# Kernel tuning notes

Measured on AMD Instinct MI355X. Metric: run time of the kernel, lower is better.

Reference implementation:

```python
import jax, jax.numpy as jnp
import jax.scipy.linalg as jsp
import numpy as np

# Problem dimensions (match init_kwargs P_shape/A_shape)
N = 256   # variables
M = 512   # constraints
B = 64    # batch

# OSQP ADMM hyper-parameters (fixed-rho variant of the OSQP algorithm)
SIGMA = 1e-6
RHO = 0.1
ALPHA = 1.6
N_ITERS = 500


def setup_inputs() -> dict:
    key = jax.random.key(0)
    kP, kq, kA, kc = jax.random.split(key, 4)
    # P is diagonal with strictly positive entries -> PSD (values are the nnz of P)
    P_val = jax.random.uniform(kP, (B, N), dtype=jnp.float32) + 0.1
    q_val = jax.random.normal(kq, (B, N), dtype=jnp.float32)
    # A is a dense pattern; values stored row-major as its nnz vector
    A_val = jax.random.normal(kA, (B, M * N), dtype=jnp.float32) / np.sqrt(N)
    # Feasible box: l <= u by construction
    center = jax.random.normal(kc, (B, M), dtype=jnp.float32)
    l_val = center - 1.0
    u_val = center + 1.0
    return {"P_val": P_val, "q_val": q_val, "A_val": A_val, "l_val": l_val, "u_val": u_val}


def _admm_qp(P_val, q_val, A_val, l_val, u_val):
    """Batched OSQP-style ADMM solve of min 1/2 x'Px + q'x  s.t. l <= Ax <= u.

    P is diagonal (nnz pattern = diag), A is dense (nnz pattern = full m x n).
    """
    A = A_val.reshape(B, M, N)                      # [B,m,n]
    # KKT-like matrix M_k = P + sigma*I + rho*A'A   [B,n,n]
    eye = jnp.eye(N, dtype=P_val.dtype)
    P_diag = P_val + SIGMA                          # diagonal of P + sigma*I
    Mk = RHO * jnp.einsum('bmi,bmj->bij', A, A) + jax.vmap(jnp.diag)(P_diag)
    L = jnp.linalg.cholesky(Mk)                     # [B,n,n], factor once, reuse
    Lt = jnp.swapaxes(L, -1, -2)

    def kkt_solve(rhs):                             # rhs [B,n]
        y1 = jsp.solve_triangular(L, rhs[..., None], lower=True)
        y2 = jsp.solve_triangular(Lt, y1, lower=False)
        return y2[..., 0]

    x0 = jnp.zeros((B, N), dtype=P_val.dtype)
    z0 = jnp.zeros((B, M), dtype=P_val.dtype)
    y0 = jnp.zeros((B, M), dtype=P_val.dtype)

    def step(state, _):
        x, z, y = state
        rhs = SIGMA * x - q_val + jnp.einsum('bmn,bm->bn', A, RHO * z - y)
        x_t = kkt_solve(rhs)                        # x-tilde
        z_t = jnp.einsum('bmn,bn->bm', A, x_t)      # z-tilde = A x_t
        x_new = ALPHA * x_t + (1.0 - ALPHA) * x
        z_hat = ALPHA * z_t + (1.0 - ALPHA) * z
        z_new = jnp.clip(z_hat + y / RHO, l_val, u_val)
        y_new = y + RHO * (z_hat - z_new)
        return (x_new, z_new, y_new), None

    (x, _, _), _ = jax.lax.scan(step, (x0, z0, y0), None, length=N_ITERS)
    return x


def reference(P_val, q_val, A_val, l_val, u_val):
    return _admm_qp(P_val, q_val, A_val, l_val, u_val)   # [B, n] primal solutions
```

## Files before the change

### kernel.cpp

```cpp
#include <hip/hip_runtime.h>
#include <hip/hip_fp16.h>

#define N_VAR 256
#define M_CON 512
#define BATCH 64
#define SIGMA_C 1e-6f
#define RHO_C 0.1f
#define ALPHA_C 1.6f
#define NITERS 500

__global__ __launch_bounds__(256) void k_transpose(const float* __restrict__ A,
                                                   float* __restrict__ At) {
  __shared__ float tile[32][33];
  int b = blockIdx.z;
  int n0 = blockIdx.x * 32;
  int m0 = blockIdx.y * 32;
  const float* Ab = A + (size_t)b * (M_CON * N_VAR);
  float* Atb = At + (size_t)b * (M_CON * N_VAR);
  int tx = threadIdx.x, ty = threadIdx.y;
#pragma unroll
  for (int j = 0; j < 32; j += 8)
    tile[ty + j][tx] = Ab[(size_t)(m0 + ty + j) * N_VAR + n0 + tx];
  __syncthreads();
#pragma unroll
  for (int j = 0; j < 32; j += 8)
    Atb[(size_t)(n0 + ty + j) * M_CON + m0 + tx] = tile[tx][ty + j];
}

__global__ __launch_bounds__(256) void k_ntgemm(
    const float* __restrict__ X, const float* __restrict__ Y,
    float* __restrict__ C, int I, int J, int K,
    long long bsX, long long bsY, long long bsC, float alpha,
    const float* __restrict__ diagv, int tilesJ) {
  int b = blockIdx.y;
  int ti = blockIdx.x / tilesJ, tj = blockIdx.x % tilesJ;
  int i0 = ti * 128, j0 = tj * 128;
  const float* Xb = X + (size_t)b * bsX;
  const float* Yb = Y + (size_t)b * bsY;
  float* Cb = C + (size_t)b * bsC;
  __shared__ float Xs[16][128];
  __shared__ float Ys[16][128];
  int tid = threadIdx.x;
  int tx = tid & 15, ty = tid >> 4;
  float acc[8][8];
#pragma unroll
  for (int r = 0; r < 8; ++r)
#pragma unroll
    for (int c = 0; c < 8; ++c) acc[r][c] = 0.0f;

  for (int kk = 0; kk < K; kk += 16) {
#pragma unroll
    for (int v = 0; v < 2; ++v) {
      int idx = v * 256 + tid;
      int row = idx >> 2;
      int k4 = (idx & 3) * 4;
      float4 gx = *(const float4*)(Xb + (size_t)(i0 + row) * K + kk + k4);
      Xs[k4 + 0][row] = gx.x; Xs[k4 + 1][row] = gx.y;
      Xs[k4 + 2][row] = gx.z; Xs[k4 + 3][row] = gx.w;
      float4 gy = *(const float4*)(Yb + (size_t)(j0 + row) * K + kk + k4);
      Ys[k4 + 0][row] = gy.x; Ys[k4 + 1][row] = gy.y;
      Ys[k4 + 2][row] = gy.z; Ys[k4 + 3][row] = gy.w;
    }
    __syncthreads();
#pragma unroll
    for (int k = 0; k < 16; ++k) {
      float xr[8], yr[8];
      *(float4*)&xr[0] = *(float4*)&Xs[k][ty * 8];
      *(float4*)&xr[4] = *(float4*)&Xs[k][ty * 8 + 4];
      *(float4*)&yr[0] = *(float4*)&Ys[k][tx * 8];
      *(float4*)&yr[4] = *(float4*)&Ys[k][tx * 8 + 4];
#pragma unroll
      for (int r = 0; r < 8; ++r)
#pragma unroll
        for (int c = 0; c < 8; ++c) acc[r][c] += xr[r] * yr[c];
    }
    __syncthreads();
  }
#pragma unroll
  for (int r = 0; r < 8; ++r) {
    int gi = i0 + ty * 8 + r;
#pragma unroll
    for (int c = 0; c < 8; ++c) {
      int gj = j0 + tx * 8 + c;
      float val = acc[r][c] * alpha;
      if (diagv != nullptr && gi == gj) val += diagv[(size_t)b * N_VAR + gi] + SIGMA_C;
      Cb[(size_t)gi * J + gj] = val;
    }
  }
}

__global__ __launch_bounds__(512, 2) void k_invert(const float* __restrict__ Mk,
                                                   float* __restrict__ Mi) {
  int b = blockIdx.x;
  const float* src = Mk + (size_t)b * 65536;
  float* dst = Mi + (size_t)b * 65536;
  int t = threadIdx.x;
  int c = t & 255, rh = t >> 8;

  float a[128];
#pragma unroll
  for (int j = 0; j < 128; ++j) a[j] = src[(size_t)(rh * 128 + j) * 256 + c];

  __shared__ float colPan[256][8];
  __shared__ float rowPan[2][8][260];
  __shared__ float PiSh[64];
  __shared__ float Rp[8][260];

  int rh_s = __builtin_amdgcn_readfirstlane(rh);
  int cw_s = __builtin_amdgcn_readfirstlane((t >> 6) & 3);

  if (rh == 0) {
#pragma unroll
    for (int j = 0; j < 8; ++j) rowPan[0][j][c] = a[j];
  }
  __syncthreads();

  for (int s = 0; s < 32; ++s) {
    int kb = s * 8;
    int cur = s & 1, nxt = cur ^ 1;
    int kh = kb >> 7, kj = kb & 127;
    int khn = (kb + 8) >> 7, kjn = (kb + 8) & 127;
    bool mycol = (c >= kb) && (c < kb + 8);

    if (cw_s == (kb >> 6)) {
      if (mycol) {
        int f = c - kb;
#pragma unroll
        for (int j = 0; j < 128; ++j) colPan[rh * 128 + j][f] = a[j];
      }
    }
    if (t < 64) {
      int e = t >> 3, f = t & 7;
      float p = rowPan[cur][e][kb + f];
#pragma unroll
      for (int k2 = 0; k2 < 8; ++k2) {
        float piv = __shfl(p, k2 * 8 + k2);
        float rv = __shfl(p, k2 * 8 + f);
        float cv = __shfl(p, e * 8 + k2);
        float pivinv = 1.0f / piv;
        float srv = rv * pivinv;
        float gen = p - cv * srv;
        p = gen;
        if (e == k2) p = srv;
        if (f == k2) p = -cv * pivinv;
        if (e == k2 && f == k2) p = pivinv;
      }
      PiSh[t] = p;
    }
    __syncthreads();

    float rpan[8];
#pragma unroll
    for (int f2 = 0; f2 < 8; ++f2) rpan[f2] = rowPan[cur][f2][c];
    float rp[8];
#pragma unroll
    for (int e = 0; e < 8; ++e) {
      float4 p0 = *(const float4*)&PiSh[e * 8];
      float4 p1 = *(const float4*)&PiSh[e * 8 + 4];
      rp[e] = p0.x * rpan[0] + p0.y * rpan[1] + p0.z * rpan[2] + p0.w * rpan[3] +
              p1.x * rpan[4] + p1.y * rpan[5] + p1.z * rpan[6] + p1.w * rpan[7];
    }
    if (cw_s == (kb >> 6)) {
      if (mycol) {
        int f = c - kb;
#pragma unroll
        for (int e = 0; e < 8; ++e) rp[e] = PiSh[e * 8 + f];
      }
    }
#pragma unroll
    for (int e = 0; e < 8; ++e) Rp[e][c] = rp[e];

    bool myhalfk = (rh_s == kh);
    bool stashw = (s != 31) && (rh_s == khn);
#pragma unroll
    for (int j = 0; j < 128; ++j) {
      float4 c0 = *(const float4*)&colPan[rh * 128 + j][0];
      float4 c1 = *(const float4*)&colPan[rh * 128 + j][4];
      float aold = a[j];
      float nv = aold -
                 (c0.x * rp[0] + c0.y * rp[1] + c0.z * rp[2] + c0.w * rp[3] +
                  c1.x * rp[4] + c1.y * rp[5] + c1.z * rp[6] + c1.w * rp[7]);
      if (mycol) nv -= aold;
      if (myhalfk && j >= kj && j < kj + 8)
        nv = Rp[j - kj][c];
      a[j] = nv;
      if (stashw && j >= kjn && j < kjn + 8)
        rowPan[nxt][j - kjn][c] = nv;
    }
    __syncthreads();
  }

#pragma unroll
  for (int j = 0; j < 128; ++j) dst[(size_t)(rh * 128 + j) * 256 + c] = a[j];
}

__global__ __launch_bounds__(256) void k_matvec_h(const float* __restrict__ Mi,
                                                  const float* __restrict__ q,
                                                  float* __restrict__ h) {
  int b = blockIdx.x, t = threadIdx.x;
  __shared__ float qs[256];
  qs[t] = q[(size_t)b * 256 + t];
  __syncthreads();
  const float* Mb = Mi + (size_t)b * 65536;
  float acc = 0.0f;
  for (int k = 0; k < 256; ++k) acc += Mb[(size_t)k * 256 + t] * qs[k];
  h[(size_t)b * 256 + t] = acc;
}

__global__ __launch_bounds__(512) void k_matvec_d(const float* __restrict__ At,
                                                  const float* __restrict__ h,
                                                  float* __restrict__ d) {
  int b = blockIdx.x, t = threadIdx.x;
  __shared__ float hs[256];
  if (t < 256) hs[t] = h[(size_t)b * 256 + t];
  __syncthreads();
  const float* Ab = At + (size_t)b * 131072;
  float acc = 0.0f;
  for (int n = 0; n < 256; ++n) acc += Ab[(size_t)n * 512 + t] * hs[n];
  d[(size_t)b * 512 + t] = acc;
}

__global__ __launch_bounds__(512, 2) void k_admm4(
    const float* __restrict__ G, const float* __restrict__ dvec,
    const float* __restrict__ lv, const float* __restrict__ uv,
    unsigned long long* __restrict__ wtag, float* __restrict__ Sbuf) {
  int g = blockIdx.x;
  int b = (g & 7) + 8 * ((g >> 3) & 7);
  int s = g >> 6;
  int t = threadIdx.x;
  int l = t & 63, wv = t >> 6;
  int c0 = wv * 64;

  __shared__ __align__(16) float wbuf[8][64];
  __shared__ float part[2][8][128];

  const float* Gb = G + (size_t)b * 262144;
  const float* g0p = Gb + (size_t)(s * 128 + l) * 512 + c0;
  const float* g1p = Gb + (size_t)(s * 128 + 64 + l) * 512 + c0;
  float G0[64], G1[64];
#pragma unroll
  for (int j = 0; j < 16; ++j) {
    float4 v0 = *(const float4*)(g0p + 4 * j);
    G0[4 * j + 0] = v0.x; G0[4 * j + 1] = v0.y;
    G0[4 * j + 2] = v0.z; G0[4 * j + 3] = v0.w;
    float4 v1 = *(const float4*)(g1p + 4 * j);
    G1[4 * j + 0] = v1.x; G1[4 * j + 1] = v1.y;
    G1[4 * j + 2] = v1.z; G1[4 * j + 3] = v1.w;
  }

  float zreg = 0.0f, yreg = 0.0f, Sreg = 0.0f;
  float lreg = 0.0f, ureg = 0.0f, dreg = 0.0f;
  if (t < 128) {
    lreg = lv[(size_t)b * 512 + s * 128 + t];
    ureg = uv[(size_t)b * 512 + s * 128 + t];
    dreg = dvec[(size_t)b * 512 + s * 128 + t];
  }
  wbuf[wv][l] = 0.0f;

  unsigned long long* wt0 = wtag + (size_t)b * 512;
  unsigned long long* wt1 = wtag + 32768 + (size_t)b * 512;
  const float4* wq4 = (const float4*)(wbuf[wv]);

  for (int it = 0; it < NITERS; ++it) {
    if (it > 0) {
      unsigned long long* wp = (it & 1) ? wt1 : wt0;
      unsigned want = (unsigned)it;
      unsigned long long v;
      for (;;) {
        v = __hip_atomic_load(&wp[c0 + l], __ATOMIC_RELAXED,
                              __HIP_MEMORY_SCOPE_AGENT);
        if (__all((unsigned)(v >> 32) == want)) break;
        __builtin_amdgcn_s_sleep(1);
      }
      wbuf[wv][l] = __uint_as_float((unsigned)(v & 0xffffffffu));
    }

    float r0a = 0.f, r0b = 0.f, r1a = 0.f, r1b = 0.f;
#pragma unroll
    for (int j = 0; j < 8; ++j) {
      float4 wa = wq4[2 * j];
      float4 wc = wq4[2 * j + 1];
      r0a += G0[8 * j + 0] * wa.x + G0[8 * j + 1] * wa.y +
             G0[8 * j + 2] * wa.z + G0[8 * j + 3] * wa.w;
      r1a += G1[8 * j + 0] * wa.x + G1[8 * j + 1] * wa.y +
             G1[8 * j + 2] * wa.z + G1[8 * j + 3] * wa.w;
      r0b += G0[8 * j + 4] * wc.x + G0[8 * j + 5] * wc.y +
             G0[8 * j + 6] * wc.z + G0[8 * j + 7] * wc.w;
      r1b += G1[8 * j + 4] * wc.x + G1[8 * j + 5] * wc.y +
             G1[8 * j + 6] * wc.z + G1[8 * j + 7] * wc.w;
    }
    int pp = it & 1;
    part[pp][wv][l] = r0a + r0b;
    part[pp][wv][64 + l] = r1a + r1b;
    __syncthreads();

    if (t < 128) {
      float w_old = RHO_C * zreg - yreg;
      Sreg = w_old - 0.6f * Sreg;
      float p = part[pp][0][t] + part[pp][1][t] + part[pp][2][t] +
                part[pp][3][t] + part[pp][4][t] + part[pp][5][t] +
                part[pp][6][t] + part[pp][7][t];
      float zt = p - dreg;
      float zh = ALPHA_C * zt + (1.0f - ALPHA_C) * zreg;
      float zc = zh + yreg * (1.0f / RHO_C);
      zc = fminf(fmaxf(zc, lreg), ureg);
      yreg += RHO_C * (zh - zc);
      zreg = zc;
      if (it < NITERS - 1) {
        float wn = RHO_C * zreg - yreg;
        unsigned long long pk =
            ((unsigned long long)(unsigned)(it + 1) << 32) |
            (unsigned long long)__float_as_uint(wn);
        unsigned long long* wp = ((it + 1) & 1) ? wt1 : wt0;
        __hip_atomic_store(&wp[s * 128 + t], pk, __ATOMIC_RELAXED,
                           __HIP_MEMORY_SCOPE_AGENT);
      }
    }
  }

  if (t < 128) Sbuf[(size_t)b * 512 + s * 128 + t] = Sreg;
}

__global__ __launch_bounds__(256) void k_final(
    const float* __restrict__ A, const float* __restrict__ q,
    const float* __restrict__ Mi, const float* __restrict__ Sbuf,
    float* __restrict__ xout) {
  int b = blockIdx.x, t = threadIdx.x;
  __shared__ float Ssh[512];
  __shared__ float uu[256];
  for (int i = t; i < 512; i += 256) Ssh[i] = Sbuf[(size_t)b * 512 + i];
  __syncthreads();
  const float* Ab = A + (size_t)b * 131072;
  float acc = 0.0f;
  for (int m = 0; m < 512; ++m) acc += Ab[(size_t)m * 256 + t] * Ssh[m];
  uu[t] = ALPHA_C * acc - q[(size_t)b * 256 + t];
  __syncthreads();
  const float* Mb = Mi + (size_t)b * 65536;
  float x = 0.0f;
  for (int kk = 0; kk < 256; ++kk) x += Mb[(size_t)kk * 256 + t] * uu[kk];
  xout[(size_t)b * 256 + t] = x;
}

extern "C" void kernel_launch(void* const* d_in, const int* in_sizes, int n_in,
                              void* d_out, int out_size, void* d_ws, size_t ws_size,
                              hipStream_t stream) {
  (void)in_sizes; (void)n_in; (void)out_size; (void)ws_size;
  const float* P = (const float*)d_in[0];
  const float* q = (const float*)d_in[1];
  const float* Av = (const float*)d_in[2];
  const float* lv = (const float*)d_in[3];
  const float* uv = (const float*)d_in[4];
  float* xout = (float*)d_out;

  float* ws = (float*)d_ws;
  float* At = ws;
  float* F  = ws;
  float* Mi = ws + 8388608;
  float* Mk = ws + 12582912;
  float* G  = ws + 12582912;
  float* hv = ws + 29360128;
  float* dv = ws + 29376512;
  float* Sbuf = ws + 29409280;
  unsigned long long* wtag = (unsigned long long*)ws;

  k_transpose<<<dim3(8, 16, 64), dim3(32, 8), 0, stream>>>(Av, At);
  k_ntgemm<<<dim3(4, 64), 256, 0, stream>>>(At, At, Mk, 256, 256, 512,
                                            131072LL, 131072LL, 65536LL,
                                            RHO_C, P, 2);
  k_invert<<<64, 512, 0, stream>>>(Mk, Mi);
  k_matvec_h<<<64, 256, 0, stream>>>(Mi, q, hv);
  k_matvec_d<<<64, 512, 0, stream>>>(At, hv, dv);
  k_ntgemm<<<dim3(8, 64), 256, 0, stream>>>(Av, Mi, F, 512, 256, 256,
                                            131072LL, 65536LL, 131072LL,
                                            1.0f, nullptr, 2);
  k_ntgemm<<<dim3(16, 64), 256, 0, stream>>>(F, Av, G, 512, 512, 256,
                                             131072LL, 131072LL, 262144LL,
                                             1.0f, nullptr, 4);
  k_admm4<<<256, 512, 0, stream>>>(G, dv, lv, uv, wtag, Sbuf);
  k_final<<<64, 256, 0, stream>>>(Av, q, Mi, Sbuf, xout);
}
```

Measured before the change: 1.592 ms.

## Give each wave its own row block to remove per-iteration block barrier

Redistributes the G matrix so each wavefront owns 16 full rows (each lane holds 8 columns) instead of each wave owning a 64-column slice for all 128 rows. The per-iteration block-wide __syncthreads and cross-wave partial-sum reduction are replaced by a wave-local LDS transpose plus shuffles, so waves progress independently. Each lane now polls 8 tagged words for the w vector instead of one. This raises register use (128 floats of G per lane) and may strain occupancy under launch_bounds(512,2).

```diff
diff --git a/kernel.cpp b/kernel.cpp
--- a/kernel.cpp
+++ b/kernel.cpp
@@ -229,96 +229,108 @@
   int s = g >> 6;
   int t = threadIdx.x;
   int l = t & 63, wv = t >> 6;
-  int c0 = wv * 64;
-
-  __shared__ __align__(16) float wbuf[8][64];
-  __shared__ float part[2][8][128];
+
+  __shared__ __align__(16) float part[8][16][68];
 
   const float* Gb = G + (size_t)b * 262144;
-  const float* g0p = Gb + (size_t)(s * 128 + l) * 512 + c0;
-  const float* g1p = Gb + (size_t)(s * 128 + 64 + l) * 512 + c0;
-  float G0[64], G1[64];
-#pragma unroll
-  for (int j = 0; j < 16; ++j) {
-    float4 v0 = *(const float4*)(g0p + 4 * j);
-    G0[4 * j + 0] = v0.x; G0[4 * j + 1] = v0.y;
-    G0[4 * j + 2] = v0.z; G0[4 * j + 3] = v0.w;
-    float4 v1 = *(const float4*)(g1p + 4 * j);
-    G1[4 * j + 0] = v1.x; G1[4 * j + 1] = v1.y;
-    G1[4 * j + 2] = v1.z; G1[4 * j + 3] = v1.w;
-  }
-
+  int rbase = s * 128 + wv * 16;
+  float Greg[128];
+#pragma unroll
+  for (int r = 0; r < 16; ++r) {
+    const float* gp = Gb + (size_t)(rbase + r) * 512 + 8 * l;
+    float4 a0 = *(const float4*)(gp);
+    float4 a1 = *(const float4*)(gp + 4);
+    Greg[r * 8 + 0] = a0.x; Greg[r * 8 + 1] = a0.y;
+    Greg[r * 8 + 2] = a0.z; Greg[r * 8 + 3] = a0.w;
+    Greg[r * 8 + 4] = a1.x; Greg[r * 8 + 5] = a1.y;
+    Greg[r * 8 + 6] = a1.z; Greg[r * 8 + 7] = a1.w;
+  }
+
+  int r2 = l >> 2, q = l & 3;
+  int row_u = rbase + r2;
+  float lreg = lv[(size_t)b * 512 + row_u];
+  float ureg = uv[(size_t)b * 512 + row_u];
+  float dreg = dvec[(size_t)b * 512 + row_u];
   float zreg = 0.0f, yreg = 0.0f, Sreg = 0.0f;
-  float lreg = 0.0f, ureg = 0.0f, dreg = 0.0f;
-  if (t < 128) {
-    lreg = lv[(size_t)b * 512 + s * 128 + t];
-    ureg = uv[(size_t)b * 512 + s * 128 + t];
-    dreg = dvec[(size_t)b * 512 + s * 128 + t];
-  }
-  wbuf[wv][l] = 0.0f;
 
   unsigned long long* wt0 = wtag + (size_t)b * 512;
   unsigned long long* wt1 = wtag + 32768 + (size_t)b * 512;
-  const float4* wq4 = (const float4*)(wbuf[wv]);
+
+  float wj[8];
+#pragma unroll
+  for (int j = 0; j < 8; ++j) wj[j] = 0.0f;
 
   for (int it = 0; it < NITERS; ++it) {
     if (it > 0) {
       unsigned long long* wp = (it & 1) ? wt1 : wt0;
       unsigned want = (unsigned)it;
-      unsigned long long v;
+      unsigned long long v[8];
+#pragma unroll
+      for (int j = 0; j < 8; ++j)
+        v[j] = __hip_atomic_load(&wp[8 * l + j], __ATOMIC_RELAXED,
+                                 __HIP_MEMORY_SCOPE_AGENT);
       for (;;) {
-        v = __hip_atomic_load(&wp[c0 + l], __ATOMIC_RELAXED,
-                              __HIP_MEMORY_SCOPE_AGENT);
-        if (__all((unsigned)(v >> 32) == want)) break;
+        bool ok = true;
+#pragma unroll
+        for (int j = 0; j < 8; ++j) ok &= ((unsigned)(v[j] >> 32) == want);
+        if (__all(ok)) break;
         __builtin_amdgcn_s_sleep(1);
-      }
-      wbuf[wv][l] = __uint_as_float((unsigned)(v & 0xffffffffu));
-    }
-
-    float r0a = 0.f, r0b = 0.f, r1a = 0.f, r1b = 0.f;
-#pragma unroll
-    for (int j = 0; j < 8; ++j) {
-      float4 wa = wq4[2 * j];
-      float4 wc = wq4[2 * j + 1];
-      r0a += G0[8 * j + 0] * wa.x + G0[8 * j + 1] * wa.y +
-             G0[8 * j + 2] * wa.z + G0[8 * j + 3] * wa.w;
-      r1a += G1[8 * j + 0] * wa.x + G1[8 * j + 1] * wa.y +
-             G1[8 * j + 2] * wa.z + G1[8 * j + 3] * wa.w;
-      r0b += G0[8 * j + 4] * wc.x + G0[8 * j + 5] * wc.y +
-             G0[8 * j + 6] * wc.z + G0[8 * j + 7] * wc.w;
-      r1b += G1[8 * j + 4] * wc.x + G1[8 * j + 5] * wc.y +
-             G1[8 * j + 6] * wc.z + G1[8 * j + 7] * wc.w;
-    }
-    int pp = it & 1;
-    part[pp][wv][l] = r0a + r0b;
-    part[pp][wv][64 + l] = r1a + r1b;
-    __syncthreads();
-
-    if (t < 128) {
-      float w_old = RHO_C * zreg - yreg;
-      Sreg = w_old - 0.6f * Sreg;
-      float p = part[pp][0][t] + part[pp][1][t] + part[pp][2][t] +
-                part[pp][3][t] + part[pp][4][t] + part[pp][5][t] +
-                part[pp][6][t] + part[pp][7][t];
-      float zt = p - dreg;
-      float zh = ALPHA_C * zt + (1.0f - ALPHA_C) * zreg;
-      float zc = zh + yreg * (1.0f / RHO_C);
-      zc = fminf(fmaxf(zc, lreg), ureg);
-      yreg += RHO_C * (zh - zc);
-      zreg = zc;
-      if (it < NITERS - 1) {
-        float wn = RHO_C * zreg - yreg;
+#pragma unroll
+        for (int j = 0; j < 8; ++j)
+          if ((unsigned)(v[j] >> 32) != want)
+            v[j] = __hip_atomic_load(&wp[8 * l + j], __ATOMIC_RELAXED,
+                                     __HIP_MEMORY_SCOPE_AGENT);
+      }
+#pragma unroll
+      for (int j = 0; j < 8; ++j)
+        wj[j] = __uint_as_float((unsigned)(v[j] & 0xffffffffu));
+    }
+
+    float acc[16];
+#pragma unroll
+    for (int r = 0; r < 16; ++r) acc[r] = 0.0f;
+#pragma unroll
+    for (int j = 0; j < 8; ++j)
+#pragma unroll
+      for (int r = 0; r < 16; ++r) acc[r] += Greg[r * 8 + j] * wj[j];
+
+#pragma unroll
+    for (int r = 0; r < 16; ++r) part[wv][r][l] = acc[r];
+    const float* pr = &part[wv][r2][q * 16];
+    float4 s0 = *(const float4*)(pr);
+    float4 s1 = *(const float4*)(pr + 4);
+    float4 s2 = *(const float4*)(pr + 8);
+    float4 s3 = *(const float4*)(pr + 12);
+    float p16 = ((s0.x + s0.y) + (s0.z + s0.w)) +
+                ((s1.x + s1.y) + (s1.z + s1.w)) +
+                ((s2.x + s2.y) + (s2.z + s2.w)) +
+                ((s3.x + s3.y) + (s3.z + s3.w));
+    p16 += __shfl_xor(p16, 1);
+    p16 += __shfl_xor(p16, 2);
+
+    float w_old = RHO_C * zreg - yreg;
+    Sreg = w_old - 0.6f * Sreg;
+    float zt = p16 - dreg;
+    float zh = ALPHA_C * zt + (1.0f - ALPHA_C) * zreg;
+    float zc = zh + yreg * (1.0f / RHO_C);
+    zc = fminf(fmaxf(zc, lreg), ureg);
+    yreg += RHO_C * (zh - zc);
+    zreg = zc;
+
+    if (it < NITERS - 1) {
+      float wn = RHO_C * zreg - yreg;
+      if (q == 0) {
         unsigned long long pk =
             ((unsigned long long)(unsigned)(it + 1) << 32) |
             (unsigned long long)__float_as_uint(wn);
         unsigned long long* wp = ((it + 1) & 1) ? wt1 : wt0;
-        __hip_atomic_store(&wp[s * 128 + t], pk, __ATOMIC_RELAXED,
+        __hip_atomic_store(&wp[row_u], pk, __ATOMIC_RELAXED,
                            __HIP_MEMORY_SCOPE_AGENT);
       }
     }
   }
 
-  if (t < 128) Sbuf[(size_t)b * 512 + s * 128 + t] = Sreg;
+  if (q == 0) Sbuf[(size_t)b * 512 + row_u] = Sreg;
 }
 
 __global__ __launch_bounds__(256) void k_final(
```

Measured after the change: 4.626 ms. 191% more time.
